# Kernel optimization log

Measured on AMD Instinct MI355X. Metric: run time of the kernel, lower is better.

## Reference

```python
import jax, jax.numpy as jnp
import numpy as np

D = 1024; H = 16; K = 64; BK = 32; FFN = 4096; LORA = 48; CHUNK = 64
THETA_CLIP = float(np.pi / 2)
THETA_INIT = float(np.pi / 16)


def layernorm(x, g, b, eps=1e-6):
    m = x.mean(-1, keepdims=True)
    v = ((x - m) ** 2).mean(-1, keepdims=True)
    return (x - m) * jax.lax.rsqrt(v + eps) * g + b


def setup_inputs() -> dict:
    key = jax.random.key(0)
    ks = jax.random.split(key, 24)
    w = lambda k, s: jax.random.normal(k, s, jnp.float32) * 0.02
    return {
        "x": jax.random.normal(ks[0], (4, 2048, D), jnp.float32),
        "Wq": w(ks[1], (D, D)), "bq": jnp.zeros((D,), jnp.float32),
        "Wk": w(ks[2], (D, D)), "bk": jnp.zeros((D,), jnp.float32),
        "Wv": w(ks[3], (D, D)), "bv": jnp.zeros((D,), jnp.float32),
        "Wo": w(ks[4], (D, D)), "bo": jnp.zeros((D,), jnp.float32),
        "n1g": jnp.ones((D,), jnp.float32), "n1b": jnp.zeros((D,), jnp.float32),
        "n2g": jnp.ones((D,), jnp.float32), "n2b": jnp.zeros((D,), jnp.float32),
        "theta_base": jax.random.uniform(ks[5], (H, BK), jnp.float32, -THETA_INIT, THETA_INIT),
        "theta_w1": w(ks[6], (D, LORA)),
        "theta_w2": jax.random.uniform(ks[7], (LORA, H * BK), jnp.float32, -0.01, 0.01),
        "lambda_base": jax.random.uniform(ks[8], (H, BK), jnp.float32, 0.5, 6.0),
        "eta": jax.random.normal(ks[9], (H, BK), jnp.float32) * 0.1,
        "Wf1": w(ks[10], (D, FFN)), "bf1": jnp.zeros((FFN,), jnp.float32),
        "Wf2": w(ks[11], (FFN, D)), "bf2": jnp.zeros((D,), jnp.float32),
    }


def _forward(x, Wq, bq, Wk, bk, Wv, bv, Wo, bo, n1g, n1b, n2g, n2b,
             theta_base, theta_w1, theta_w2, lambda_base, eta, Wf1, bf1, Wf2, bf2):
    B, T, _ = x.shape
    NC = T // CHUNK
    xn = layernorm(x, n1g, n1b)
    # projections -> (B, H, T, K)
    q = (xn @ Wq + bq).reshape(B, T, H, K).transpose(0, 2, 1, 3)
    k = (xn @ Wk + bk).reshape(B, T, H, K).transpose(0, 2, 1, 3)
    v = (xn @ Wv + bv).reshape(B, T, H, K).transpose(0, 2, 1, 3)
    phi_k = jnp.where(k > 0, k + 1.0, jnp.exp(k))  # elu(k) + 1
    qp = q.reshape(B, H, T, BK, 2)
    kp = phi_k.reshape(B, H, T, BK, 2)
    q_c = jax.lax.complex(qp[..., 0], qp[..., 1])  # (B,H,T,BK) complex64
    k_c = jax.lax.complex(kp[..., 0], kp[..., 1])
    # data-dependent rotation angles via LoRA
    lora = jnp.tanh(xn @ theta_w1) @ theta_w2  # (B,T,H*BK)
    theta = theta_base[None, None] + lora.reshape(B, T, H, BK)
    theta = jnp.clip(theta, -THETA_CLIP, THETA_CLIP).transpose(0, 2, 1, 3)  # (B,H,T,BK)
    lam = lambda_base[None, :, None, :] + eta[None, :, None, :] * theta ** 2
    log_z = jax.lax.complex(-lam, theta)  # complex log-decay per step

    def chunks(a):  # (B,H,T,...) -> (NC,B,H,CHUNK,...)
        return jnp.moveaxis(a.reshape(B, H, NC, CHUNK, *a.shape[3:]), 2, 0)

    tril = jnp.tril(jnp.ones((CHUNK, CHUNK), bool))[None, None, :, :, None]

    def step(c, inputs):
        lz, kc, qc, vf = inputs  # (B,H,tc,BK)x3, (B,H,tc,K)
        cumlog = jnp.cumsum(lz, axis=2)
        diff = cumlog[:, :, :, None, :] - cumlog[:, :, None, :, :]  # (B,H,tc,tc,BK)
        real = jnp.where(tril, diff.real, -60.0)
        A = jnp.where(tril, jnp.exp(jax.lax.complex(real, diff.imag)),
                      jnp.zeros((), jnp.complex64))
        scaled_k = A * kc[:, :, None, :, :]
        S_intra = jnp.einsum('bhtsk,bhsv->bhtkv', scaled_k, vf.astype(jnp.complex64))
        decay = jnp.exp(cumlog)
        S_total = decay[..., None] * c[:, :, None] + S_intra  # (B,H,tc,BK,K)
        y = jnp.einsum('bhtk,bhtkv->bhtv', jnp.conj(qc), S_total).real
        return S_total[:, :, -1], y

    c0 = jnp.zeros((B, H, BK, K), jnp.complex64)
    _, ys = jax.lax.scan(step, c0, (chunks(log_z), chunks(k_c), chunks(q_c), chunks(v)))
    out = jnp.moveaxis(ys, 0, 2).reshape(B, H, T, K)
    attn = out.transpose(0, 2, 1, 3).reshape(B, T, D) @ Wo + bo
    x1 = x + attn
    h = layernorm(x1, n2g, n2b)
    return x1 + jax.nn.gelu(h @ Wf1 + bf1) @ Wf2 + bf2


def reference(x, Wq, bq, Wk, bk, Wv, bv, Wo, bo, n1g, n1b, n2g, n2b,
              theta_base, theta_w1, theta_w2, lambda_base, eta, Wf1, bf1, Wf2, bf2):
    return _forward(x, Wq, bq, Wk, bk, Wv, bv, Wo, bo, n1g, n1b, n2g, n2b,
                    theta_base, theta_w1, theta_w2, lambda_base, eta, Wf1, bf1, Wf2, bf2)
```

## Files before the change

### kernel.cpp

```cpp
#include <hip/hip_runtime.h>


typedef __bf16 bf16x8 __attribute__((ext_vector_type(8)));
typedef float f32x4 __attribute__((ext_vector_type(4)));

__device__ __forceinline__ unsigned short f2bf(float f) {
  unsigned int u = __builtin_bit_cast(unsigned int, f);
  u += 0x7FFFu + ((u >> 16) & 1u);
  return (unsigned short)(u >> 16);
}
__device__ __forceinline__ float bf2f(unsigned short u) {
  unsigned int x = ((unsigned int)u) << 16;
  return __builtin_bit_cast(float, x);
}
__device__ __forceinline__ unsigned int pack2(float a, float b) {
  return (unsigned int)f2bf(a) | ((unsigned int)f2bf(b) << 16);
}

__device__ __forceinline__ void gload_lds16(const void* g, void* l) {
  __builtin_amdgcn_global_load_lds((const __attribute__((address_space(1))) void*)g,
                                   (__attribute__((address_space(3))) void*)l, 16, 0, 0);
}

__device__ __forceinline__ float gelu_tanh(float v) {
  const float z = 0.7978845608028654f * fmaf(0.044715f * v * v, v, v);
  const float e = __expf(2.f * z);
  return 0.5f * v * (2.f - 2.f / (1.f + e));
}

__global__ void fill_kernel(float* p, float v, int n) {
  int i = blockIdx.x * 256 + threadIdx.x;
  if (i < n) p[i] = v;
}

__global__ __launch_bounds__(256) void ln_kernel(
    const float* __restrict__ x, const float* __restrict__ g,
    const float* __restrict__ b, unsigned short* __restrict__ out) {
  const int row = blockIdx.x, tid = threadIdx.x;
  float4 v = ((const float4*)(x + (size_t)row * 1024))[tid];
  float s = v.x + v.y + v.z + v.w;
  float sq = v.x * v.x + v.y * v.y + v.z * v.z + v.w * v.w;
#pragma unroll
  for (int o = 32; o > 0; o >>= 1) { s += __shfl_xor(s, o); sq += __shfl_xor(sq, o); }
  __shared__ float red[8];
  const int wid = tid >> 6;
  if ((tid & 63) == 0) { red[wid] = s; red[4 + wid] = sq; }
  __syncthreads();
  s = red[0] + red[1] + red[2] + red[3];
  sq = red[4] + red[5] + red[6] + red[7];
  const float mean = s * (1.f / 1024.f);
  const float var = sq * (1.f / 1024.f) - mean * mean;
  const float rstd = rsqrtf(var + 1e-6f);
  float4 gv = ((const float4*)g)[tid];
  float4 bvv = ((const float4*)b)[tid];
  ushort4 o4;
  o4.x = f2bf((v.x - mean) * rstd * gv.x + bvv.x);
  o4.y = f2bf((v.y - mean) * rstd * gv.y + bvv.y);
  o4.z = f2bf((v.z - mean) * rstd * gv.z + bvv.z);
  o4.w = f2bf((v.w - mean) * rstd * gv.w + bvv.w);
  *(ushort4*)(out + (size_t)row * 1024 + tid * 4) = o4;
}

__global__ __launch_bounds__(256) void transpose_bf16(
    const float* __restrict__ src, unsigned short* __restrict__ dst, int K, int N) {
  __shared__ float tile[32][33];
  const int n0 = blockIdx.x * 32, k0 = blockIdx.y * 32;
  const int tx = threadIdx.x, ty = threadIdx.y;
#pragma unroll
  for (int j = 0; j < 32; j += 8) tile[tx][ty + j] = src[(size_t)(k0 + ty + j) * N + n0 + tx];
  __syncthreads();
#pragma unroll
  for (int j = 0; j < 32; j += 8)
    dst[(size_t)(n0 + ty + j) * K + k0 + tx] = f2bf(tile[ty + j][tx]);
}

__global__ __launch_bounds__(256) void prep_wcat(
    const float* __restrict__ Wq, const float* __restrict__ Wk,
    const float* __restrict__ Wv, const float* __restrict__ tw1,
    unsigned short* __restrict__ dst) {
  __shared__ float tile[32][33];
  const int r0 = blockIdx.x * 32, c0 = blockIdx.y * 32;
  const int tx = threadIdx.x, ty = threadIdx.y;
  const int r = r0 + tx;
#pragma unroll
  for (int j = 0; j < 32; j += 8) {
    const int c = c0 + ty + j;
    float v;
    if (r < 1024) v = Wq[(size_t)c * 1024 + r];
    else if (r < 2048) v = Wk[(size_t)c * 1024 + (r - 1024)];
    else if (r < 3072) v = Wv[(size_t)c * 1024 + (r - 2048)];
    else if (r < 3120) v = tw1[(size_t)c * 48 + (r - 3072)];
    else v = 0.f;
    tile[tx][ty + j] = v;
  }
  __syncthreads();
#pragma unroll
  for (int j = 0; j < 32; j += 8)
    dst[(size_t)(r0 + ty + j) * 1024 + c0 + tx] = f2bf(tile[ty + j][tx]);
}

__global__ void biascat_kernel(const float* bq, const float* bk, const float* bv, float* dst) {
  int i = blockIdx.x * 256 + threadIdx.x;
  if (i >= 3200) return;
  float v = 0.f;
  if (i < 1024) v = bq[i];
  else if (i < 2048) v = bk[i - 1024];
  else if (i < 3072) v = bv[i - 2048];
  dst[i] = v;
}

template <int MODE>
__global__ __launch_bounds__(256) void gemm_kernel(
    const unsigned short* __restrict__ A, const unsigned short* __restrict__ BT,
    const float* __restrict__ bias, const float* __restrict__ res,
    void* __restrict__ out, int N, int Kd) {
  __shared__ unsigned short As[2][128 * 64];
  __shared__ unsigned short Bs[2][128 * 64];
  const int nwg = gridDim.x * gridDim.y;
  int d = blockIdx.y * gridDim.x + blockIdx.x;
  d = (d & 7) * (nwg >> 3) + (d >> 3);
  const int n0 = (d % gridDim.x) * 128, m0 = (d / gridDim.x) * 128;

  const int tid = threadIdx.x, wv = tid >> 6, ln = tid & 63;
  const int wm = wv >> 1, wn = wv & 1;
  const int l15 = ln & 15, hi4 = ln >> 4;
  const int rbase = wv * 8 + (ln >> 3);
  const int kgofs = ((ln & 7) ^ ((ln >> 3) & 7)) * 8;

  auto STAGE = [&](int buf, int k0) {
#pragma unroll
    for (int jj = 0; jj < 4; ++jj) {
      gload_lds16(A + (size_t)(m0 + jj * 32 + rbase) * Kd + k0 + kgofs,
                  (char*)&As[buf][0] + (jj * 256 + wv * 64) * 16);
      gload_lds16(BT + (size_t)(n0 + jj * 32 + rbase) * Kd + k0 + kgofs,
                  (char*)&Bs[buf][0] + (jj * 256 + wv * 64) * 16);
    }
  };

  f32x4 acc[4][4] = {};
  const int nt = Kd >> 6;
  STAGE(0, 0);
  asm volatile("s_waitcnt vmcnt(0)" ::: "memory");
  __builtin_amdgcn_s_barrier();
  __builtin_amdgcn_sched_barrier(0);
  int cur = 0;
  for (int t = 0; t < nt; ++t) {
    if (t + 1 < nt) STAGE(cur ^ 1, (t + 1) << 6);
    const unsigned short* Ac = &As[cur][0];
    const unsigned short* Bc = &Bs[cur][0];
#pragma unroll
    for (int kk = 0; kk < 64; kk += 32) {
      const int kg = (kk >> 3) + hi4;
      bf16x8 av[4], bv[4];
#pragma unroll
      for (int f = 0; f < 4; ++f) {
        const int ra = wm * 64 + f * 16 + l15;
        const int rb2 = wn * 64 + f * 16 + l15;
        av[f] = *(const bf16x8*)&Ac[(ra * 8 + (kg ^ (ra & 7))) * 8];
        bv[f] = *(const bf16x8*)&Bc[(rb2 * 8 + (kg ^ (rb2 & 7))) * 8];
      }
#pragma unroll
      for (int fm = 0; fm < 4; ++fm)
#pragma unroll
        for (int fn = 0; fn < 4; ++fn)
          acc[fm][fn] = __builtin_amdgcn_mfma_f32_16x16x32_bf16(av[fm], bv[fn], acc[fm][fn], 0, 0, 0);
    }
    if (t + 1 < nt) {
      __builtin_amdgcn_sched_barrier(0);
      asm volatile("s_waitcnt vmcnt(0)" ::: "memory");
      __builtin_amdgcn_s_barrier();
      __builtin_amdgcn_sched_barrier(0);
      cur ^= 1;
    }
  }
  const int rb = hi4 * 4;
#pragma unroll
  for (int fm = 0; fm < 4; ++fm) {
#pragma unroll
    for (int fn = 0; fn < 4; ++fn) {
      const int row = m0 + wm * 64 + fm * 16 + rb;
      const int col = n0 + wn * 64 + fn * 16 + l15;
      const float bval = bias[col];
#pragma unroll
      for (int r = 0; r < 4; ++r) {
        float v = acc[fm][fn][r] + bval;
        const size_t oi = (size_t)(row + r) * N + col;
        if constexpr (MODE == 1) v += res[oi];
        if constexpr (MODE == 2) {
          ((unsigned short*)out)[oi] = f2bf(gelu_tanh(v));
        } else if constexpr (MODE == 3) {
          ((unsigned short*)out)[oi] = f2bf(v);
        } else {
          ((float*)out)[oi] = v;
        }
      }
    }
  }
}

__global__ __launch_bounds__(256) void lora2_kernel(
    const unsigned short* __restrict__ qkv, const float* __restrict__ w2,
    const float* __restrict__ tbase, float* __restrict__ theta) {
  __shared__ float lt[8][48];
  const int m0 = blockIdx.x * 32;
  const int tid = threadIdx.x;
  const int col = tid * 2;
  const float tb0 = tbase[col], tb1 = tbase[col + 1];
  for (int grp = 0; grp < 4; ++grp) {
    const int mg = m0 + grp * 8;
    __syncthreads();
    for (int idx = tid; idx < 384; idx += 256) {
      const int tok = idx / 48, jj = idx % 48;
      lt[tok][jj] = tanhf(bf2f(qkv[(size_t)(mg + tok) * 3200 + 3072 + jj]));
    }
    __syncthreads();
    float a0[8], a1[8];
#pragma unroll
    for (int tok = 0; tok < 8; ++tok) { a0[tok] = tb0; a1[tok] = tb1; }
    for (int jj = 0; jj < 48; ++jj) {
      const float2 w = *(const float2*)&w2[(size_t)jj * 512 + col];
#pragma unroll
      for (int tok = 0; tok < 8; ++tok) {
        const float l = lt[tok][jj];
        a0[tok] = fmaf(l, w.x, a0[tok]);
        a1[tok] = fmaf(l, w.y, a1[tok]);
      }
    }
    const float CL = 1.5707963267948966f;
#pragma unroll
    for (int tok = 0; tok < 8; ++tok) {
      float c0 = fminf(fmaxf(a0[tok], -CL), CL);
      float c1 = fminf(fmaxf(a1[tok], -CL), CL);
      *(float2*)&theta[(size_t)(mg + tok) * 512 + col] = make_float2(c0, c1);
    }
  }
}

__global__ __launch_bounds__(256) void attn_intra(
    const unsigned short* __restrict__ qkv, const float* __restrict__ theta,
    const float* __restrict__ lamb, const float* __restrict__ eta,
    float* __restrict__ yi, unsigned short* __restrict__ QG,
    unsigned short* __restrict__ TCG, float* __restrict__ Dg) {
  const int c = blockIdx.x, bh = blockIdx.y;
  const int b = bh >> 4, h = bh & 15;
  const int tid = threadIdx.x, wv = tid >> 6, lane = tid & 63;
  const int sc = c * 4 + wv;
  const int cid = bh * 128 + sc;
  const int mw = b * 2048 + sc * 16;

  __shared__ unsigned short QDm[4][16][64];
  __shared__ unsigned short KDm[4][16][64];
  __shared__ unsigned short KdET[4][64][32];
  __shared__ unsigned short VT[4][64][32];
  __shared__ unsigned short Gs[4][16][32];

  {
    unsigned int* kz = (unsigned int*)&KdET[wv][0][0];
    unsigned int* vz = (unsigned int*)&VT[wv][0][0];
    for (int idx = lane; idx < 512; idx += 64) {
      const int r = idx >> 3, p = (idx & 7) + 8;
      kz[r * 16 + p] = 0; vz[r * 16 + p] = 0;
    }
    unsigned int* gz = (unsigned int*)&Gs[wv][0][0];
    for (int idx = lane; idx < 128; idx += 64) {
      const int r = idx >> 3, p = (idx & 7) + 8;
      gz[r * 16 + p] = 0;
    }
  }
  for (int ss = 0; ss < 16; ++ss)
    VT[wv][lane][ss] = qkv[(size_t)(mw + ss) * 3200 + 2048 + h * 64 + lane];

  const int bk = lane & 31, th = lane >> 5;
  const float lb = lamb[h * 32 + bk], et = eta[h * 32 + bk];
  float L[8], Th[8], qr[8], qi[8], kr[8], ki[8];
  float runL = 0.f, runT = 0.f;
#pragma unroll
  for (int i = 0; i < 8; ++i) {
    const size_t m = (size_t)(mw + th * 8 + i);
    const float tv = theta[m * 512 + h * 32 + bk];
    const float lam = fmaf(et * tv, tv, lb);
    runL += lam; L[i] = runL;
    runT += tv;  Th[i] = runT;
    const unsigned int qp = *(const unsigned int*)&qkv[m * 3200 + h * 64 + 2 * bk];
    const unsigned int kp = *(const unsigned int*)&qkv[m * 3200 + 1024 + h * 64 + 2 * bk];
    qr[i] = bf2f((unsigned short)(qp & 0xFFFF)); qi[i] = bf2f((unsigned short)(qp >> 16));
    const float kx = bf2f((unsigned short)(kp & 0xFFFF));
    const float ky = bf2f((unsigned short)(kp >> 16));
    kr[i] = kx > 0.f ? kx + 1.f : __expf(kx);
    ki[i] = ky > 0.f ? ky + 1.f : __expf(ky);
  }
  const float oL = __shfl_xor(runL, 32), oT = __shfl_xor(runT, 32);
  const float Lm = th ? oL : runL;
  const float Tm = th ? oT : runT;
  const float Ltot = runL + oL, Ttot = runT + oT;
  const float Lbase = th ? oL : 0.f, Tbase = th ? oT : 0.f;
  float Es, Ec; __sincosf(Tm, &Es, &Ec);
  const float Ee = __expf(-Lm);
  const float Er = Ee * Ec, Ei = Ee * Es;
  float Fs, Fc; __sincosf(Ttot - Tm, &Fs, &Fc);
  const float Fe = __expf(-(Ltot - Lm));
  const float Fr = Fe * Fc, Fi = Fe * Fs;
  if (th == 0) {
    float Ds, Dc; __sincosf(Ttot, &Ds, &Dc);
    const float De = __expf(-Ltot);
    *(float2*)&Dg[((size_t)cid * 32 + bk) * 2] = make_float2(De * Dc, De * Ds);
  }
  unsigned int* qd32 = (unsigned int*)&QDm[wv][0][0];
  unsigned int* kd32 = (unsigned int*)&KDm[wv][0][0];
#pragma unroll
  for (int i = 0; i < 8; ++i) {
    const int t = th * 8 + i;
    const float Lg = Lbase + L[i], Tg = Tbase + Th[i];
    const float dm = __expf(-(Lg - Lm));
    float sn, cs; __sincosf(Tg - Tm, &sn, &cs);
    const float qmr = dm * (qr[i] * cs + qi[i] * sn);
    const float qmi = dm * (qr[i] * sn - qi[i] * cs);
    const float rd = 1.f / dm;
    const float kmr = rd * (kr[i] * cs + ki[i] * sn);
    const float kmi = rd * (ki[i] * cs - kr[i] * sn);
    const int sidx = (t * 32 + bk) ^ ((t & 7) << 2);
    qd32[sidx] = pack2(qmr, qmi);
    kd32[sidx] = pack2(kmr, -kmi);
    ((unsigned int*)QG)[(size_t)cid * 512 + t * 32 + bk] =
        pack2(qmr * Er - qmi * Ei, qmr * Ei + qmi * Er);
    const float er = kmr * Fr - kmi * Fi;
    const float ei = kmr * Fi + kmi * Fr;
    KdET[wv][bk][t] = f2bf(er);
    KdET[wv][32 + bk][t] = f2bf(ei);
  }

  const int l15 = lane & 15, hi = lane >> 4;
  const char* qb = (const char*)&QDm[wv][0][0];
  const char* kb = (const char*)&KDm[wv][0][0];
  f32x4 z = {};
  f32x4 g = z;
  {
    bf16x8 a0 = *(const bf16x8*)(qb + l15 * 128 + ((16 * hi) ^ ((l15 & 7) << 4)));
    bf16x8 b0 = *(const bf16x8*)(kb + l15 * 128 + ((16 * hi) ^ ((l15 & 7) << 4)));
    bf16x8 a1 = *(const bf16x8*)(qb + l15 * 128 + ((64 + 16 * hi) ^ ((l15 & 7) << 4)));
    bf16x8 b1 = *(const bf16x8*)(kb + l15 * 128 + ((64 + 16 * hi) ^ ((l15 & 7) << 4)));
    g = __builtin_amdgcn_mfma_f32_16x16x32_bf16(a0, b0, g, 0, 0, 0);
    g = __builtin_amdgcn_mfma_f32_16x16x32_bf16(a1, b1, g, 0, 0, 0);
  }
#pragma unroll
  for (int r = 0; r < 4; ++r) {
    const float gv = (l15 <= 4 * hi + r) ? g[r] : 0.f;
    Gs[wv][4 * hi + r][l15] = f2bf(gv);
  }
  const char* gsb = (const char*)&Gs[wv][0][0];
  const char* vtb = (const char*)&VT[wv][0][0];
  bf16x8 aG = *(const bf16x8*)(gsb + l15 * 64 + 16 * hi);
#pragma unroll
  for (int nt = 0; nt < 4; ++nt) {
    bf16x8 bV = *(const bf16x8*)(vtb + (nt * 16 + l15) * 64 + 16 * hi);
    f32x4 y = __builtin_amdgcn_mfma_f32_16x16x32_bf16(aG, bV, z, 0, 0, 0);
#pragma unroll
    for (int r = 0; r < 4; ++r)
      yi[(size_t)cid * 1024 + (4 * hi + r) * 64 + nt * 16 + l15] = y[r];
  }
  const char* keb = (const char*)&KdET[wv][0][0];
#pragma unroll
  for (int mt = 0; mt < 4; ++mt) {
    bf16x8 aT = *(const bf16x8*)(keb + (mt * 16 + l15) * 64 + 16 * hi);
#pragma unroll
    for (int nt = 0; nt < 4; ++nt) {
      bf16x8 bV = *(const bf16x8*)(vtb + (nt * 16 + l15) * 64 + 16 * hi);
      f32x4 t4 = __builtin_amdgcn_mfma_f32_16x16x32_bf16(aT, bV, z, 0, 0, 0);
#pragma unroll
      for (int r = 0; r < 4; ++r)
        TCG[(size_t)cid * 4096 + (mt * 16 + 4 * hi + r) * 64 + nt * 16 + l15] = f2bf(t4[r]);
    }
  }
}

__global__ __launch_bounds__(256) void scanB_kernel(
    unsigned short* __restrict__ TCG, const float* __restrict__ Dg) {
  const int bh = blockIdx.x;
  const int tid = threadIdx.x, wv = tid >> 6, lane = tid & 63;
  const int bkb = wv * 8;
  float Cr[8], Ci[8];
#pragma unroll
  for (int i = 0; i < 8; ++i) { Cr[i] = 0.f; Ci[i] = 0.f; }
  for (int c0 = 0; c0 < 128; c0 += 2) {
    float tr[2][8], ti[2][8]; float2 dv[2][8];
#pragma unroll
    for (int u = 0; u < 2; ++u) {
      const size_t cid = (size_t)bh * 128 + c0 + u;
#pragma unroll
      for (int i = 0; i < 8; ++i) {
        tr[u][i] = bf2f(TCG[cid * 4096 + (bkb + i) * 64 + lane]);
        ti[u][i] = bf2f(TCG[cid * 4096 + (32 + bkb + i) * 64 + lane]);
        dv[u][i] = *(const float2*)&Dg[(cid * 32 + bkb + i) * 2];
      }
    }
    __syncthreads();
#pragma unroll
    for (int u = 0; u < 2; ++u) {
      const size_t cid = (size_t)bh * 128 + c0 + u;
#pragma unroll
      for (int i = 0; i < 8; ++i) {
        ((unsigned int*)TCG)[cid * 2048 + (size_t)lane * 32 + bkb + i] = pack2(Cr[i], -Ci[i]);
        const float nr = fmaf(dv[u][i].x, Cr[i], fmaf(-dv[u][i].y, Ci[i], tr[u][i]));
        const float ni = fmaf(dv[u][i].x, Ci[i], fmaf(dv[u][i].y, Cr[i], ti[u][i]));
        Cr[i] = nr; Ci[i] = ni;
      }
    }
  }
}

__global__ __launch_bounds__(256) void attn_cross(
    const float* __restrict__ yi, const unsigned short* __restrict__ QG,
    const unsigned short* __restrict__ TCG, unsigned short* __restrict__ attn) {
  const int c = blockIdx.x, bh = blockIdx.y;
  const int b = bh >> 4, h = bh & 15;
  const int tid = threadIdx.x, wv = tid >> 6, lane = tid & 63;
  const int sc = c * 4 + wv, cid = bh * 128 + sc;
  const int mw = b * 2048 + sc * 16;
  __shared__ unsigned short Cp[4][64][64];
  __shared__ unsigned short Qs[4][16][64];
  unsigned int* cp32 = (unsigned int*)&Cp[wv][0][0];
  const unsigned int* cg = (const unsigned int*)TCG + (size_t)cid * 2048;
  for (int ii = 0; ii < 32; ++ii) {
    const int flat = ii * 64 + lane;
    const int row = flat >> 5, col = flat & 31;
    cp32[(row * 32 + col) ^ ((row & 7) << 2)] = cg[flat];
  }
  unsigned int* qs32 = (unsigned int*)&Qs[wv][0][0];
  const unsigned int* qg = (const unsigned int*)QG + (size_t)cid * 512;
  for (int ii = 0; ii < 8; ++ii) {
    const int flat = ii * 64 + lane;
    const int row = flat >> 5, col = flat & 31;
    qs32[(row * 32 + col) ^ ((row & 7) << 2)] = qg[flat];
  }
  const int l15 = lane & 15, hi = lane >> 4;
  const char* qb = (const char*)&Qs[wv][0][0];
  const char* cb = (const char*)&Cp[wv][0][0];
  bf16x8 a0 = *(const bf16x8*)(qb + l15 * 128 + ((16 * hi) ^ ((l15 & 7) << 4)));
  bf16x8 a1 = *(const bf16x8*)(qb + l15 * 128 + ((64 + 16 * hi) ^ ((l15 & 7) << 4)));
  f32x4 z = {};
#pragma unroll
  for (int nt = 0; nt < 4; ++nt) {
    const int vr = nt * 16 + l15;
    bf16x8 b0 = *(const bf16x8*)(cb + vr * 128 + ((16 * hi) ^ ((vr & 7) << 4)));
    bf16x8 b1 = *(const bf16x8*)(cb + vr * 128 + ((64 + 16 * hi) ^ ((vr & 7) << 4)));
    f32x4 y = __builtin_amdgcn_mfma_f32_16x16x32_bf16(a0, b0, z, 0, 0, 0);
    y = __builtin_amdgcn_mfma_f32_16x16x32_bf16(a1, b1, y, 0, 0, 0);
#pragma unroll
    for (int r = 0; r < 4; ++r) {
      const int t = 4 * hi + r;
      const float out = y[r] + yi[(size_t)cid * 1024 + t * 64 + vr];
      attn[(size_t)(mw + t) * 1024 + h * 64 + vr] = f2bf(out);
    }
  }
}

extern "C" void kernel_launch(void* const* d_in, const int* in_sizes, int n_in,
                              void* d_out, int out_size, void* d_ws, size_t ws_size,
                              hipStream_t stream) {
  const float* x   = (const float*)d_in[0];
  const float* Wq  = (const float*)d_in[1];
  const float* bq  = (const float*)d_in[2];
  const float* Wk  = (const float*)d_in[3];
  const float* bk_ = (const float*)d_in[4];
  const float* Wv  = (const float*)d_in[5];
  const float* bv  = (const float*)d_in[6];
  const float* Wo  = (const float*)d_in[7];
  const float* bo  = (const float*)d_in[8];
  const float* n1g = (const float*)d_in[9];
  const float* n1b = (const float*)d_in[10];
  const float* n2g = (const float*)d_in[11];
  const float* n2b = (const float*)d_in[12];
  const float* thb = (const float*)d_in[13];
  const float* tw1 = (const float*)d_in[14];
  const float* tw2 = (const float*)d_in[15];
  const float* lamb= (const float*)d_in[16];
  const float* eta = (const float*)d_in[17];
  const float* Wf1 = (const float*)d_in[18];
  const float* bf1 = (const float*)d_in[19];
  const float* Wf2 = (const float*)d_in[20];
  const float* bf2 = (const float*)d_in[21];

  char* ws = (char*)d_ws;
  size_t off = 0;
  auto alloc = [&](size_t bytes) {
    size_t r = off;
    off += (bytes + 255) & ~(size_t)255;
    return r;
  };
  unsigned short* WCAT = (unsigned short*)(ws + alloc(3200ull * 1024 * 2));
  unsigned short* WOT  = (unsigned short*)(ws + alloc(1024ull * 1024 * 2));
  unsigned short* WF1T = (unsigned short*)(ws + alloc(4096ull * 1024 * 2));
  unsigned short* WF2T = (unsigned short*)(ws + alloc(1024ull * 4096 * 2));
  float* BIASC = (float*)(ws + alloc(3200ull * 4));
  unsigned short* XN = (unsigned short*)(ws + alloc(8192ull * 1024 * 2));
  char* QKVbase = ws + alloc(8192ull * 4096 * 2);
  unsigned short* QKV = (unsigned short*)QKVbase;
  unsigned short* GBUF = (unsigned short*)QKVbase;
  float* THETA = (float*)(ws + alloc(8192ull * 512 * 4));
  unsigned short* ATTN = (unsigned short*)THETA;
  float* YI = (float*)(ws + alloc(8192ull * 1024 * 4));
  float* X1 = YI;
  unsigned short* QG = (unsigned short*)(ws + alloc(8192ull * 1024 * 2));
  unsigned short* TCG = (unsigned short*)(ws + alloc(8192ull * 4096 * 2));
  float* DG = (float*)(ws + alloc(8192ull * 32 * 2 * 4));

  if (ws_size < off) {
    fill_kernel<<<dim3((out_size + 255) / 256), dim3(256), 0, stream>>>((float*)d_out, 12345.0f, out_size);
    return;
  }

  const dim3 b256(256), b32x8(32, 8);

  prep_wcat<<<dim3(100, 32), b32x8, 0, stream>>>(Wq, Wk, Wv, tw1, WCAT);
  transpose_bf16<<<dim3(32, 32), b32x8, 0, stream>>>(Wo, WOT, 1024, 1024);
  transpose_bf16<<<dim3(128, 32), b32x8, 0, stream>>>(Wf1, WF1T, 1024, 4096);
  transpose_bf16<<<dim3(32, 128), b32x8, 0, stream>>>(Wf2, WF2T, 4096, 1024);
  biascat_kernel<<<dim3(13), b256, 0, stream>>>(bq, bk_, bv, BIASC);

  ln_kernel<<<dim3(8192), b256, 0, stream>>>(x, n1g, n1b, XN);
  gemm_kernel<3><<<dim3(25, 64), b256, 0, stream>>>(XN, WCAT, BIASC, nullptr, QKV, 3200, 1024);
  lora2_kernel<<<dim3(256), b256, 0, stream>>>(QKV, tw2, thb, THETA);
  attn_intra<<<dim3(32, 64), b256, 0, stream>>>(QKV, THETA, lamb, eta, YI, QG, TCG, DG);
  scanB_kernel<<<dim3(64), b256, 0, stream>>>(TCG, DG);
  attn_cross<<<dim3(32, 64), b256, 0, stream>>>(YI, QG, TCG, ATTN);
  gemm_kernel<1><<<dim3(8, 64), b256, 0, stream>>>(ATTN, WOT, bo, x, X1, 1024, 1024);
  ln_kernel<<<dim3(8192), b256, 0, stream>>>(X1, n2g, n2b, XN);
  gemm_kernel<2><<<dim3(32, 64), b256, 0, stream>>>(XN, WF1T, bf1, nullptr, GBUF, 4096, 1024);
  gemm_kernel<1><<<dim3(8, 64), b256, 0, stream>>>(GBUF, WF2T, bf2, X1, d_out, 1024, 4096);
}
```

Baseline: 526.5 us.

## Add 256x256 pipelined GEMM and parallelize chunk scan across value columns

Introduces a 512-thread GEMM with 256x256 tiles, double-buffered direct global-to-LDS loads, XOR-swizzled LDS and a workgroup remap. It is used for the output projection and both FFN GEMMs, to raise data reuse and overlap loads with MFMA. The chunk-state scan now spreads each head's state over 8 blocks, one thread per (value, BK) element, with prefetching. It writes the packed state into a separate buffer that aliases the dead QKV region, where it used to write back into TCG in place. This exposes 8x more parallelism in a latency-bound serial scan. Risks include lower occupancy from heavy LDS and register use, and reduced wave counts for the N=1024 GEMMs (128 blocks).

```diff
diff --git a/kernel.cpp b/kernel.cpp
--- a/kernel.cpp
+++ b/kernel.cpp
@@ -192,6 +192,125 @@
           ((unsigned short*)out)[oi] = f2bf(v);
         } else {
           ((float*)out)[oi] = v;
+        }
+      }
+    }
+  }
+}
+
+template <int MODE>
+__global__ __launch_bounds__(512) void gemm256_kernel(
+    const unsigned short* __restrict__ A, const unsigned short* __restrict__ BT,
+    const float* __restrict__ bias, const float* __restrict__ res,
+    void* __restrict__ out, int N, int Kd) {
+  __shared__ __align__(16) unsigned short SA[2][2][8192];
+  __shared__ __align__(16) unsigned short SB[2][2][8192];
+  const int nwg = gridDim.x * gridDim.y;
+  int d = blockIdx.y * gridDim.x + blockIdx.x;
+  d = (d & 7) * (nwg >> 3) + (d >> 3);
+  const int n0 = (d % gridDim.x) * 256, m0 = (d / gridDim.x) * 256;
+
+  const int tid = threadIdx.x, wv = tid >> 6, ln = tid & 63;
+  const int wm = wv >> 2, wn = wv & 3;
+  const int l15 = ln & 15, hi4 = ln >> 4;
+
+  auto STAGE = [&](int p, int k0) {
+    const unsigned short* Ab = A + (size_t)m0 * Kd + k0;
+    const unsigned short* Bb = BT + (size_t)n0 * Kd + k0;
+#pragma unroll
+    for (int hf = 0; hf < 2; ++hf) {
+#pragma unroll
+      for (int r = 0; r < 2; ++r) {
+        const int slot = (r * 8 + wv) * 64 + ln;
+        const int row = slot >> 3;
+        const int kg = (slot & 7) ^ (row & 7);
+        gload_lds16(Ab + (size_t)(hf * 128 + row) * Kd + kg * 8,
+                    (char*)&SA[p][hf][0] + (r * 8 + wv) * 1024);
+        gload_lds16(Bb + (size_t)(hf * 128 + row) * Kd + kg * 8,
+                    (char*)&SB[p][hf][0] + (r * 8 + wv) * 1024);
+      }
+    }
+  };
+
+  f32x4 acc[8][4] = {};
+  const int nt = Kd >> 6;
+  STAGE(0, 0);
+  STAGE(1, 64);
+  asm volatile("s_waitcnt vmcnt(8)" ::: "memory");
+  __builtin_amdgcn_s_barrier();
+  __builtin_amdgcn_sched_barrier(0);
+
+  for (int t = 0; t < nt; ++t) {
+    const int p = t & 1;
+    const unsigned short* Ahalf = &SA[p][wm][0];
+    bf16x8 bfr[4][2];
+#pragma unroll
+    for (int q = 0; q < 4; ++q) {
+      bf16x8 af[2][2];
+#pragma unroll
+      for (int j = 0; j < 2; ++j) {
+        const int row = (2 * q + j) * 16 + l15;
+#pragma unroll
+        for (int ks = 0; ks < 2; ++ks) {
+          const int kg = ks * 4 + hi4;
+          af[j][ks] = *(const bf16x8*)&Ahalf[(row * 8 + (kg ^ (row & 7))) * 8];
+        }
+      }
+      if (q == 0) {
+#pragma unroll
+        for (int fn = 0; fn < 4; ++fn) {
+          const int nrow = wn * 64 + fn * 16 + l15;
+          const unsigned short* Bhalf = &SB[p][nrow >> 7][0];
+          const int rowin = nrow & 127;
+#pragma unroll
+          for (int ks = 0; ks < 2; ++ks) {
+            const int kg = ks * 4 + hi4;
+            bfr[fn][ks] = *(const bf16x8*)&Bhalf[(rowin * 8 + (kg ^ (rowin & 7))) * 8];
+          }
+        }
+      }
+      __builtin_amdgcn_s_setprio(1);
+#pragma unroll
+      for (int j = 0; j < 2; ++j)
+#pragma unroll
+        for (int fn = 0; fn < 4; ++fn)
+#pragma unroll
+          for (int ks = 0; ks < 2; ++ks)
+            acc[2 * q + j][fn] =
+                __builtin_amdgcn_mfma_f32_16x16x32_bf16(af[j][ks], bfr[fn][ks], acc[2 * q + j][fn], 0, 0, 0);
+      __builtin_amdgcn_s_setprio(0);
+    }
+    __builtin_amdgcn_sched_barrier(0);
+    __builtin_amdgcn_s_barrier();
+    __builtin_amdgcn_sched_barrier(0);
+    if (t + 2 < nt) {
+      STAGE(p, (t + 2) << 6);
+      __builtin_amdgcn_sched_barrier(0);
+      asm volatile("s_waitcnt vmcnt(8)" ::: "memory");
+    } else if (t + 1 < nt) {
+      asm volatile("s_waitcnt vmcnt(0)" ::: "memory");
+    }
+    if (t + 1 < nt) {
+      __builtin_amdgcn_s_barrier();
+      __builtin_amdgcn_sched_barrier(0);
+    }
+  }
+
+#pragma unroll
+  for (int fm = 0; fm < 8; ++fm) {
+#pragma unroll
+    for (int fn = 0; fn < 4; ++fn) {
+      const int row = m0 + wm * 128 + fm * 16 + hi4 * 4;
+      const int col = n0 + wn * 64 + fn * 16 + l15;
+      const float bval = bias[col];
+#pragma unroll
+      for (int r = 0; r < 4; ++r) {
+        float v = acc[fm][fn][r] + bval;
+        const size_t oi = (size_t)(row + r) * N + col;
+        if constexpr (MODE == 1) {
+          ((float*)out)[oi] = v + res[oi];
+        } else {
+          ((unsigned short*)out)[oi] = f2bf(gelu_tanh(v));
         }
       }
     }
@@ -374,43 +493,42 @@
 }
 
 __global__ __launch_bounds__(256) void scanB_kernel(
-    unsigned short* __restrict__ TCG, const float* __restrict__ Dg) {
-  const int bh = blockIdx.x;
-  const int tid = threadIdx.x, wv = tid >> 6, lane = tid & 63;
-  const int bkb = wv * 8;
-  float Cr[8], Ci[8];
-#pragma unroll
-  for (int i = 0; i < 8; ++i) { Cr[i] = 0.f; Ci[i] = 0.f; }
-  for (int c0 = 0; c0 < 128; c0 += 2) {
-    float tr[2][8], ti[2][8]; float2 dv[2][8];
-#pragma unroll
-    for (int u = 0; u < 2; ++u) {
-      const size_t cid = (size_t)bh * 128 + c0 + u;
-#pragma unroll
-      for (int i = 0; i < 8; ++i) {
-        tr[u][i] = bf2f(TCG[cid * 4096 + (bkb + i) * 64 + lane]);
-        ti[u][i] = bf2f(TCG[cid * 4096 + (32 + bkb + i) * 64 + lane]);
-        dv[u][i] = *(const float2*)&Dg[(cid * 32 + bkb + i) * 2];
-      }
-    }
-    __syncthreads();
-#pragma unroll
-    for (int u = 0; u < 2; ++u) {
-      const size_t cid = (size_t)bh * 128 + c0 + u;
-#pragma unroll
-      for (int i = 0; i < 8; ++i) {
-        ((unsigned int*)TCG)[cid * 2048 + (size_t)lane * 32 + bkb + i] = pack2(Cr[i], -Ci[i]);
-        const float nr = fmaf(dv[u][i].x, Cr[i], fmaf(-dv[u][i].y, Ci[i], tr[u][i]));
-        const float ni = fmaf(dv[u][i].x, Ci[i], fmaf(dv[u][i].y, Cr[i], ti[u][i]));
-        Cr[i] = nr; Ci[i] = ni;
-      }
+    const unsigned short* __restrict__ TCG, const float* __restrict__ Dg,
+    unsigned int* __restrict__ CPACK) {
+  const int bh = blockIdx.x & 63, g = blockIdx.x >> 6;
+  const int tid = threadIdx.x;
+  const int v = g * 8 + (tid >> 5), bk = tid & 31;
+  const size_t base = (size_t)bh * 128;
+  float Cr = 0.f, Ci = 0.f;
+  float trx[4], tix[4]; float2 dx[4];
+  auto LOADQ = [&](int c0, float* tr, float* ti, float2* dd) {
+#pragma unroll
+    for (int u = 0; u < 4; ++u) {
+      const size_t cid = base + c0 + u;
+      tr[u] = bf2f(TCG[cid * 4096 + bk * 64 + v]);
+      ti[u] = bf2f(TCG[cid * 4096 + (32 + bk) * 64 + v]);
+      dd[u] = *(const float2*)&Dg[(cid * 32 + bk) * 2];
+    }
+  };
+  LOADQ(0, trx, tix, dx);
+  for (int c0 = 0; c0 < 128; c0 += 4) {
+    float tra[4], tia[4]; float2 da[4];
+#pragma unroll
+    for (int u = 0; u < 4; ++u) { tra[u] = trx[u]; tia[u] = tix[u]; da[u] = dx[u]; }
+    if (c0 + 4 < 128) LOADQ(c0 + 4, trx, tix, dx);
+#pragma unroll
+    for (int u = 0; u < 4; ++u) {
+      CPACK[(base + c0 + u) * 2048 + v * 32 + bk] = pack2(Cr, -Ci);
+      const float nr = fmaf(da[u].x, Cr, fmaf(-da[u].y, Ci, tra[u]));
+      const float ni = fmaf(da[u].x, Ci, fmaf(da[u].y, Cr, tia[u]));
+      Cr = nr; Ci = ni;
     }
   }
 }
 
 __global__ __launch_bounds__(256) void attn_cross(
     const float* __restrict__ yi, const unsigned short* __restrict__ QG,
-    const unsigned short* __restrict__ TCG, unsigned short* __restrict__ attn) {
+    const unsigned int* __restrict__ CPACK, unsigned short* __restrict__ attn) {
   const int c = blockIdx.x, bh = blockIdx.y;
   const int b = bh >> 4, h = bh & 15;
   const int tid = threadIdx.x, wv = tid >> 6, lane = tid & 63;
@@ -419,7 +537,7 @@
   __shared__ unsigned short Cp[4][64][64];
   __shared__ unsigned short Qs[4][16][64];
   unsigned int* cp32 = (unsigned int*)&Cp[wv][0][0];
-  const unsigned int* cg = (const unsigned int*)TCG + (size_t)cid * 2048;
+  const unsigned int* cg = CPACK + (size_t)cid * 2048;
   for (int ii = 0; ii < 32; ++ii) {
     const int flat = ii * 64 + lane;
     const int row = flat >> 5, col = flat & 31;
@@ -495,6 +613,7 @@
   unsigned short* XN = (unsigned short*)(ws + alloc(8192ull * 1024 * 2));
   char* QKVbase = ws + alloc(8192ull * 4096 * 2);
   unsigned short* QKV = (unsigned short*)QKVbase;
+  unsigned int* CPACK = (unsigned int*)QKVbase;
   unsigned short* GBUF = (unsigned short*)QKVbase;
   float* THETA = (float*)(ws + alloc(8192ull * 512 * 4));
   unsigned short* ATTN = (unsigned short*)THETA;
@@ -509,7 +628,7 @@
     return;
   }
 
-  const dim3 b256(256), b32x8(32, 8);
+  const dim3 b256(256), b32x8(32, 8), b512(512);
 
   prep_wcat<<<dim3(100, 32), b32x8, 0, stream>>>(Wq, Wk, Wv, tw1, WCAT);
   transpose_bf16<<<dim3(32, 32), b32x8, 0, stream>>>(Wo, WOT, 1024, 1024);
@@ -521,10 +640,10 @@
   gemm_kernel<3><<<dim3(25, 64), b256, 0, stream>>>(XN, WCAT, BIASC, nullptr, QKV, 3200, 1024);
   lora2_kernel<<<dim3(256), b256, 0, stream>>>(QKV, tw2, thb, THETA);
   attn_intra<<<dim3(32, 64), b256, 0, stream>>>(QKV, THETA, lamb, eta, YI, QG, TCG, DG);
-  scanB_kernel<<<dim3(64), b256, 0, stream>>>(TCG, DG);
-  attn_cross<<<dim3(32, 64), b256, 0, stream>>>(YI, QG, TCG, ATTN);
-  gemm_kernel<1><<<dim3(8, 64), b256, 0, stream>>>(ATTN, WOT, bo, x, X1, 1024, 1024);
+  scanB_kernel<<<dim3(512), b256, 0, stream>>>(TCG, DG, CPACK);
+  attn_cross<<<dim3(32, 64), b256, 0, stream>>>(YI, QG, CPACK, ATTN);
+  gemm256_kernel<1><<<dim3(4, 32), b512, 0, stream>>>(ATTN, WOT, bo, x, X1, 1024, 1024);
   ln_kernel<<<dim3(8192), b256, 0, stream>>>(X1, n2g, n2b, XN);
-  gemm_kernel<2><<<dim3(32, 64), b256, 0, stream>>>(XN, WF1T, bf1, nullptr, GBUF, 4096, 1024);
-  gemm_kernel<1><<<dim3(8, 64), b256, 0, stream>>>(GBUF, WF2T, bf2, X1, d_out, 1024, 4096);
-}
+  gemm256_kernel<2><<<dim3(16, 32), b512, 0, stream>>>(XN, WF1T, bf1, nullptr, GBUF, 4096, 1024);
+  gemm256_kernel<1><<<dim3(4, 32), b512, 0, stream>>>(GBUF, WF2T, bf2, X1, d_out, 1024, 4096);
+}
```

Measured after the change: 572.7 us. +8.8%, slower.

## Parallelise chunk-state scan across value columns and drop GEMM double buffering

Applied to the files above, without the earlier changes.

The cross-chunk scan kernel goes from 64 blocks, each handling a full 32x64 state per batch-head, to 512 blocks where each thread carries one (bk, v) complex state. Loads are prefetched four chunks ahead, and results go to a separate CPACK buffer aliased onto the QKV region instead of overwriting TCG in place. This is meant to remove the low-occupancy serial scan bottleneck. Separately, the GEMM kernel's double-buffered LDS pipeline is replaced by a single buffer with __syncthreads before and after each K-step. That halves shared memory per block, possibly allowing more resident blocks, but loses the overlap of global loads with MFMA work.

```diff
diff --git a/kernel.cpp b/kernel.cpp
--- a/kernel.cpp
+++ b/kernel.cpp
@@ -114,8 +114,8 @@
     const unsigned short* __restrict__ A, const unsigned short* __restrict__ BT,
     const float* __restrict__ bias, const float* __restrict__ res,
     void* __restrict__ out, int N, int Kd) {
-  __shared__ unsigned short As[2][128 * 64];
-  __shared__ unsigned short Bs[2][128 * 64];
+  __shared__ unsigned short As[128 * 64];
+  __shared__ unsigned short Bs[128 * 64];
   const int nwg = gridDim.x * gridDim.y;
   int d = blockIdx.y * gridDim.x + blockIdx.x;
   d = (d & 7) * (nwg >> 3) + (d >> 3);
@@ -127,27 +127,16 @@
   const int rbase = wv * 8 + (ln >> 3);
   const int kgofs = ((ln & 7) ^ ((ln >> 3) & 7)) * 8;
 
-  auto STAGE = [&](int buf, int k0) {
+  f32x4 acc[4][4] = {};
+  for (int k0 = 0; k0 < Kd; k0 += 64) {
 #pragma unroll
     for (int jj = 0; jj < 4; ++jj) {
       gload_lds16(A + (size_t)(m0 + jj * 32 + rbase) * Kd + k0 + kgofs,
-                  (char*)&As[buf][0] + (jj * 256 + wv * 64) * 16);
+                  (char*)As + (jj * 256 + wv * 64) * 16);
       gload_lds16(BT + (size_t)(n0 + jj * 32 + rbase) * Kd + k0 + kgofs,
-                  (char*)&Bs[buf][0] + (jj * 256 + wv * 64) * 16);
-    }
-  };
-
-  f32x4 acc[4][4] = {};
-  const int nt = Kd >> 6;
-  STAGE(0, 0);
-  asm volatile("s_waitcnt vmcnt(0)" ::: "memory");
-  __builtin_amdgcn_s_barrier();
-  __builtin_amdgcn_sched_barrier(0);
-  int cur = 0;
-  for (int t = 0; t < nt; ++t) {
-    if (t + 1 < nt) STAGE(cur ^ 1, (t + 1) << 6);
-    const unsigned short* Ac = &As[cur][0];
-    const unsigned short* Bc = &Bs[cur][0];
+                  (char*)Bs + (jj * 256 + wv * 64) * 16);
+    }
+    __syncthreads();
 #pragma unroll
     for (int kk = 0; kk < 64; kk += 32) {
       const int kg = (kk >> 3) + hi4;
@@ -156,8 +145,8 @@
       for (int f = 0; f < 4; ++f) {
         const int ra = wm * 64 + f * 16 + l15;
         const int rb2 = wn * 64 + f * 16 + l15;
-        av[f] = *(const bf16x8*)&Ac[(ra * 8 + (kg ^ (ra & 7))) * 8];
-        bv[f] = *(const bf16x8*)&Bc[(rb2 * 8 + (kg ^ (rb2 & 7))) * 8];
+        av[f] = *(const bf16x8*)&As[(ra * 8 + (kg ^ (ra & 7))) * 8];
+        bv[f] = *(const bf16x8*)&Bs[(rb2 * 8 + (kg ^ (rb2 & 7))) * 8];
       }
 #pragma unroll
       for (int fm = 0; fm < 4; ++fm)
@@ -165,13 +154,7 @@
         for (int fn = 0; fn < 4; ++fn)
           acc[fm][fn] = __builtin_amdgcn_mfma_f32_16x16x32_bf16(av[fm], bv[fn], acc[fm][fn], 0, 0, 0);
     }
-    if (t + 1 < nt) {
-      __builtin_amdgcn_sched_barrier(0);
-      asm volatile("s_waitcnt vmcnt(0)" ::: "memory");
-      __builtin_amdgcn_s_barrier();
-      __builtin_amdgcn_sched_barrier(0);
-      cur ^= 1;
-    }
+    __syncthreads();
   }
   const int rb = hi4 * 4;
 #pragma unroll
@@ -374,43 +357,42 @@
 }
 
 __global__ __launch_bounds__(256) void scanB_kernel(
-    unsigned short* __restrict__ TCG, const float* __restrict__ Dg) {
-  const int bh = blockIdx.x;
-  const int tid = threadIdx.x, wv = tid >> 6, lane = tid & 63;
-  const int bkb = wv * 8;
-  float Cr[8], Ci[8];
-#pragma unroll
-  for (int i = 0; i < 8; ++i) { Cr[i] = 0.f; Ci[i] = 0.f; }
-  for (int c0 = 0; c0 < 128; c0 += 2) {
-    float tr[2][8], ti[2][8]; float2 dv[2][8];
-#pragma unroll
-    for (int u = 0; u < 2; ++u) {
-      const size_t cid = (size_t)bh * 128 + c0 + u;
-#pragma unroll
-      for (int i = 0; i < 8; ++i) {
-        tr[u][i] = bf2f(TCG[cid * 4096 + (bkb + i) * 64 + lane]);
-        ti[u][i] = bf2f(TCG[cid * 4096 + (32 + bkb + i) * 64 + lane]);
-        dv[u][i] = *(const float2*)&Dg[(cid * 32 + bkb + i) * 2];
-      }
-    }
-    __syncthreads();
-#pragma unroll
-    for (int u = 0; u < 2; ++u) {
-      const size_t cid = (size_t)bh * 128 + c0 + u;
-#pragma unroll
-      for (int i = 0; i < 8; ++i) {
-        ((unsigned int*)TCG)[cid * 2048 + (size_t)lane * 32 + bkb + i] = pack2(Cr[i], -Ci[i]);
-        const float nr = fmaf(dv[u][i].x, Cr[i], fmaf(-dv[u][i].y, Ci[i], tr[u][i]));
-        const float ni = fmaf(dv[u][i].x, Ci[i], fmaf(dv[u][i].y, Cr[i], ti[u][i]));
-        Cr[i] = nr; Ci[i] = ni;
-      }
+    const unsigned short* __restrict__ TCG, const float* __restrict__ Dg,
+    unsigned int* __restrict__ CPACK) {
+  const int bh = blockIdx.x & 63, g = blockIdx.x >> 6;
+  const int tid = threadIdx.x;
+  const int v = g * 8 + (tid >> 5), bk = tid & 31;
+  const size_t base = (size_t)bh * 128;
+  float Cr = 0.f, Ci = 0.f;
+  float trx[4], tix[4]; float2 dx[4];
+  auto LOADQ = [&](int c0, float* tr, float* ti, float2* dd) {
+#pragma unroll
+    for (int u = 0; u < 4; ++u) {
+      const size_t cid = base + c0 + u;
+      tr[u] = bf2f(TCG[cid * 4096 + bk * 64 + v]);
+      ti[u] = bf2f(TCG[cid * 4096 + (32 + bk) * 64 + v]);
+      dd[u] = *(const float2*)&Dg[(cid * 32 + bk) * 2];
+    }
+  };
+  LOADQ(0, trx, tix, dx);
+  for (int c0 = 0; c0 < 128; c0 += 4) {
+    float tra[4], tia[4]; float2 da[4];
+#pragma unroll
+    for (int u = 0; u < 4; ++u) { tra[u] = trx[u]; tia[u] = tix[u]; da[u] = dx[u]; }
+    if (c0 + 4 < 128) LOADQ(c0 + 4, trx, tix, dx);
+#pragma unroll
+    for (int u = 0; u < 4; ++u) {
+      CPACK[(base + c0 + u) * 2048 + v * 32 + bk] = pack2(Cr, -Ci);
+      const float nr = fmaf(da[u].x, Cr, fmaf(-da[u].y, Ci, tra[u]));
+      const float ni = fmaf(da[u].x, Ci, fmaf(da[u].y, Cr, tia[u]));
+      Cr = nr; Ci = ni;
     }
   }
 }
 
 __global__ __launch_bounds__(256) void attn_cross(
     const float* __restrict__ yi, const unsigned short* __restrict__ QG,
-    const unsigned short* __restrict__ TCG, unsigned short* __restrict__ attn) {
+    const unsigned int* __restrict__ CPACK, unsigned short* __restrict__ attn) {
   const int c = blockIdx.x, bh = blockIdx.y;
   const int b = bh >> 4, h = bh & 15;
   const int tid = threadIdx.x, wv = tid >> 6, lane = tid & 63;
@@ -419,7 +401,7 @@
   __shared__ unsigned short Cp[4][64][64];
   __shared__ unsigned short Qs[4][16][64];
   unsigned int* cp32 = (unsigned int*)&Cp[wv][0][0];
-  const unsigned int* cg = (const unsigned int*)TCG + (size_t)cid * 2048;
+  const unsigned int* cg = CPACK + (size_t)cid * 2048;
   for (int ii = 0; ii < 32; ++ii) {
     const int flat = ii * 64 + lane;
     const int row = flat >> 5, col = flat & 31;
@@ -495,6 +477,7 @@
   unsigned short* XN = (unsigned short*)(ws + alloc(8192ull * 1024 * 2));
   char* QKVbase = ws + alloc(8192ull * 4096 * 2);
   unsigned short* QKV = (unsigned short*)QKVbase;
+  unsigned int* CPACK = (unsigned int*)QKVbase;
   unsigned short* GBUF = (unsigned short*)QKVbase;
   float* THETA = (float*)(ws + alloc(8192ull * 512 * 4));
   unsigned short* ATTN = (unsigned short*)THETA;
@@ -521,8 +504,8 @@
   gemm_kernel<3><<<dim3(25, 64), b256, 0, stream>>>(XN, WCAT, BIASC, nullptr, QKV, 3200, 1024);
   lora2_kernel<<<dim3(256), b256, 0, stream>>>(QKV, tw2, thb, THETA);
   attn_intra<<<dim3(32, 64), b256, 0, stream>>>(QKV, THETA, lamb, eta, YI, QG, TCG, DG);
-  scanB_kernel<<<dim3(64), b256, 0, stream>>>(TCG, DG);
-  attn_cross<<<dim3(32, 64), b256, 0, stream>>>(YI, QG, TCG, ATTN);
+  scanB_kernel<<<dim3(512), b256, 0, stream>>>(TCG, DG, CPACK);
+  attn_cross<<<dim3(32, 64), b256, 0, stream>>>(YI, QG, CPACK, ATTN);
   gemm_kernel<1><<<dim3(8, 64), b256, 0, stream>>>(ATTN, WOT, bo, x, X1, 1024, 1024);
   ln_kernel<<<dim3(8192), b256, 0, stream>>>(X1, n2g, n2b, XN);
   gemm_kernel<2><<<dim3(32, 64), b256, 0, stream>>>(XN, WF1T, bf1, nullptr, GBUF, 4096, 1024);
```

After: 520.9 us. About the same (-1.1%).
